# Kernel optimization log

Hardware: AMD Instinct MI355X
Metric: run time of the kernel (lower is better)

Reference implementation:

```python
import jax, jax.numpy as jnp
import numpy as np

N, Tq, Tk = 4096, 48, 48
E, H = 64, 4
HD = E // H
TN = 288            # time_num (5-min slots per day)
FE = 4              # forward_expansion
EPS = 1e-5


def _ln(x, g, b):
    mu = jnp.mean(x, axis=-1, keepdims=True)
    var = jnp.var(x, axis=-1, keepdims=True)
    return (x - mu) * jax.lax.rsqrt(var + EPS) * g + b


def setup_inputs() -> dict:
    rng = jax.random.key(0)
    ks = jax.random.split(rng, 12)
    s = 0.05
    return {
        "value": jax.random.normal(ks[0], (N, Tk, E), jnp.float32),
        "keys": jax.random.normal(ks[1], (N, Tk, E), jnp.float32),
        "query": jax.random.normal(ks[2], (N, Tq, E), jnp.float32),
        "Wv": jax.random.normal(ks[3], (HD, HD), jnp.float32) * s,
        "Wk": jax.random.normal(ks[4], (HD, HD), jnp.float32) * s,
        "Wq": jax.random.normal(ks[5], (HD, HD), jnp.float32) * s,
        "Wo": jax.random.normal(ks[6], (E, E), jnp.float32) * s,
        "bo": jnp.zeros((E,), jnp.float32),
        "temb": jax.random.normal(ks[7], (TN, E), jnp.float32) * s,
        "ln1_g": jnp.ones((E,), jnp.float32),
        "ln1_b": jnp.zeros((E,), jnp.float32),
        "ln2_g": jnp.ones((E,), jnp.float32),
        "ln2_b": jnp.zeros((E,), jnp.float32),
        "W1": jax.random.normal(ks[8], (FE * E, E), jnp.float32) * s,  # torch Linear(E, FE*E).weight
        "b1": jnp.zeros((FE * E,), jnp.float32),
        "W2": jax.random.normal(ks[9], (E, FE * E), jnp.float32) * s,
        "b2": jnp.zeros((E,), jnp.float32),
        "tq": 10,
    }


def reference(value, keys, query, Wv, Wk, Wq, Wo, bo, temb,
              ln1_g, ln1_b, ln2_g, ln2_b, W1, b1, W2, b2, tq):
    # temporal embedding add (tk = tq since tk=-1 default)
    tq_inds = (TN + tq + jnp.arange(Tq)) % TN
    tk_inds = (TN + tq + jnp.arange(Tk)) % TN
    q = query + temb[tq_inds][None, :, :]   # (N,Tq,E)
    k = keys + temb[tk_inds][None, :, :]    # (N,Tk,E)

    qh = q.reshape(N, Tq, H, HD)
    kh = k.reshape(N, Tk, H, HD)
    vh = value.reshape(N, Tk, H, HD)
    # per-head small linear projections (x @ W.T, no bias)
    qh = jnp.einsum('nthd,ed->nthe', qh, Wq)
    kh = jnp.einsum('nthd,ed->nthe', kh, Wk)
    vh = jnp.einsum('nthd,ed->nthe', vh, Wv)

    energy = jnp.einsum('nqhd,nkhd->nqkh', qh, kh)  # (N,Tq,Tk,H)
    # causal mask (mask=True path): masked entries set to -1e6 BEFORE scale+clamp
    tmask = jnp.tril(jnp.ones((Tq, Tk), jnp.float32))
    energy = jnp.where(tmask[None, :, :, None] == 0, jnp.float32(-1e6), energy)
    logits = jnp.clip(energy / jnp.float32(np.sqrt(E)), -5.0, 5.0)
    attention = jax.nn.softmax(logits, axis=2)       # softmax over k

    out = jnp.einsum('nqkh,nkhd->nqhd', attention, vh).reshape(N, Tq, E)
    out = out @ Wo.T + bo

    x = _ln(out + q, ln1_g, ln1_b)                   # dropout is identity (eval)
    ff = jax.nn.relu(x @ W1.T + b1) @ W2.T + b2
    return _ln(ff + x, ln2_g, ln2_b)
```

## Files before the change

kernel.cpp:

```cpp
#include <hip/hip_runtime.h>
#include <hip/hip_bf16.h>
#include <math.h>

#define NSEQ 4096
#define TN 288
#define EPSF 1e-5f

typedef short bf16x8 __attribute__((ext_vector_type(8)));
typedef float f32x4 __attribute__((ext_vector_type(4)));

#define WSV 0
#define WSK 256
#define WSQ 512
#define WSO 768
#define WS1 4864
#define WS2 21248

#define A_S   0
#define B_S   3456
#define C_S   6912
#define D_S   10496
#define CD_F  3456
#define H_S   6912

__device__ __forceinline__ unsigned short f2bf_u(float f) {
    __hip_bfloat16 h = __float2bfloat16(f);
    return *reinterpret_cast<const unsigned short*>(&h);
}
__device__ __forceinline__ unsigned int pk2(float a, float b) {
    return (unsigned int)f2bf_u(a) | ((unsigned int)f2bf_u(b) << 16);
}
__device__ __forceinline__ float bits2f(unsigned int u) { return __uint_as_float(u); }

__global__ void wconv_kernel(const float* __restrict__ Wv, const float* __restrict__ Wk,
                             const float* __restrict__ Wq, const float* __restrict__ Wo,
                             const float* __restrict__ W1, const float* __restrict__ W2,
                             short* __restrict__ ws) {
    int i = blockIdx.x * 256 + threadIdx.x;
    float v;
    if (i < 256)        v = Wv[i];
    else if (i < 512)   v = Wk[i - 256];
    else if (i < 768)   v = Wq[i - 512] * 0.125f;
    else if (i < 4864)  v = Wo[i - 768];
    else if (i < 21248) v = W1[i - 4864];
    else                v = W2[i - 21248];
    ws[i] = (short)f2bf_u(v);
}

__global__ __launch_bounds__(256, 5)
void ttrans_kernel(const float* __restrict__ value,
                   const float* __restrict__ keys,
                   const float* __restrict__ query,
                   const float* __restrict__ bo,
                   const float* __restrict__ temb,
                   const float* __restrict__ ln1g,
                   const float* __restrict__ ln1b,
                   const float* __restrict__ ln2g,
                   const float* __restrict__ ln2b,
                   const float* __restrict__ pb1,
                   const float* __restrict__ pb2,
                   const short* __restrict__ ws,
                   const int* __restrict__ tqp,
                   float* __restrict__ out)
{
    __shared__ __align__(16) unsigned char smem[27136];
    short* S16 = reinterpret_cast<short*>(smem);
    float* S32 = reinterpret_cast<float*>(smem);

    const int tid  = threadIdx.x;
    const int lane = tid & 63;
    const int w    = tid >> 6;
    const int l15  = lane & 15;
    const int lg   = lane >> 4;
    const int n    = blockIdx.x;
    const size_t gbase = (size_t)n * 3072;
    const int tqv  = *tqp;
    const int c4   = (lane & 15) * 4;
    const int rg   = lane >> 4;
    const int hh   = w;

    float4 qres4[3];
    {
        int t = w * 12 + rg;
        int ti = ((tqv % TN) + TN + t) % TN;
        #pragma unroll
        for (int it = 0; it < 3; ++it) {
            float4 tv = *reinterpret_cast<const float4*>(&temb[ti * 64 + c4]);
            float4 qv = *reinterpret_cast<const float4*>(&query[gbase + t * 64 + c4]);
            float4 kv = *reinterpret_cast<const float4*>(&keys [gbase + t * 64 + c4]);
            float4 vv = *reinterpret_cast<const float4*>(&value[gbase + t * 64 + c4]);
            float4 qq = make_float4(qv.x + tv.x, qv.y + tv.y, qv.z + tv.z, qv.w + tv.w);
            float4 kk = make_float4(kv.x + tv.x, kv.y + tv.y, kv.z + tv.z, kv.w + tv.w);
            qres4[it] = qq;
            *reinterpret_cast<uint2*>(&S16[A_S + t * 72 + c4]) =
                make_uint2(pk2(qq.x, qq.y), pk2(qq.z, qq.w));
            *reinterpret_cast<uint2*>(&S16[B_S + t * 72 + c4]) =
                make_uint2(pk2(kk.x, kk.y), pk2(kk.z, kk.w));
            *reinterpret_cast<uint2*>(&S16[C_S + t * 72 + c4]) =
                make_uint2(pk2(vv.x, vv.y), pk2(vv.z, vv.w));
            t += 4; ti += 4; if (ti >= TN) ti -= TN;
        }
    }
    __syncthreads();

    {
        bf16x8 bWv = {}, bWk = {}, bWq = {};
        if (lane < 32) {
            bWv = *reinterpret_cast<const bf16x8*>(&ws[WSV + l15 * 16 + lg * 8]);
            bWk = *reinterpret_cast<const bf16x8*>(&ws[WSK + l15 * 16 + lg * 8]);
            bWq = *reinterpret_cast<const bf16x8*>(&ws[WSQ + l15 * 16 + lg * 8]);
        }
        #pragma unroll
        for (int rt = 0; rt < 3; ++rt) {
            bf16x8 aQ = {}, aK = {}, aV = {};
            if (lane < 32) {
                int ro = (rt * 16 + l15) * 72 + hh * 16 + lg * 8;
                aQ = *reinterpret_cast<const bf16x8*>(&S16[A_S + ro]);
                aK = *reinterpret_cast<const bf16x8*>(&S16[B_S + ro]);
                aV = *reinterpret_cast<const bf16x8*>(&S16[C_S + ro]);
            }
            f32x4 z = {0.f,0.f,0.f,0.f};
            f32x4 cQ = __builtin_amdgcn_mfma_f32_16x16x32_bf16(aQ, bWq, z, 0, 0, 0);
            f32x4 cK = __builtin_amdgcn_mfma_f32_16x16x32_bf16(aK, bWk, z, 0, 0, 0);
            f32x4 cV = __builtin_amdgcn_mfma_f32_16x16x32_bf16(aV, bWv, z, 0, 0, 0);
            #pragma unroll
            for (int r = 0; r < 4; ++r) {
                int row = rt * 16 + lg * 4 + r;
                S16[A_S + row * 72 + hh * 16 + l15] = (short)f2bf_u(cQ[r]);
                S16[B_S + row * 72 + hh * 16 + l15] = (short)f2bf_u(cK[r]);
                S16[D_S + (hh * 16 + l15) * 48 + row] = (short)f2bf_u(cV[r]);
            }
        }
    }

    {
        const float PEXP = 0.006737946999085467f;
        const unsigned short PBF = f2bf_u(PEXP);
        bf16x8 bK0 = {}, bK1 = {}, bK2 = {};
        if (lane < 32) {
            bK0 = *reinterpret_cast<const bf16x8*>(&S16[B_S + ( 0 + l15) * 72 + hh * 16 + lg * 8]);
            bK1 = *reinterpret_cast<const bf16x8*>(&S16[B_S + (16 + l15) * 72 + hh * 16 + lg * 8]);
            bK2 = *reinterpret_cast<const bf16x8*>(&S16[B_S + (32 + l15) * 72 + hh * 16 + lg * 8]);
        }
        bf16x8 vA = *reinterpret_cast<const bf16x8*>(&S16[D_S + (hh * 16 + l15) * 48 + lg * 8]);
        bf16x8 vB = {};
        if (lane < 32)
            vB = *reinterpret_cast<const bf16x8*>(&S16[D_S + (hh * 16 + l15) * 48 + 32 + lg * 8]);
        asm volatile("" ::: "memory");

        const int abase = D_S + hh * 768;
        #pragma unroll
        for (int rt = 0; rt < 3; ++rt) {
            bf16x8 aQ = {};
            if (lane < 32)
                aQ = *reinterpret_cast<const bf16x8*>(&S16[A_S + (rt * 16 + l15) * 72 + hh * 16 + lg * 8]);
            f32x4 z = {0.f,0.f,0.f,0.f};
            f32x4 e0 = __builtin_amdgcn_mfma_f32_16x16x32_bf16(aQ, bK0, z, 0, 0, 0);
            f32x4 e1 = z, e2 = z;
            if (rt >= 1) e1 = __builtin_amdgcn_mfma_f32_16x16x32_bf16(aQ, bK1, z, 0, 0, 0);
            if (rt == 2) e2 = __builtin_amdgcn_mfma_f32_16x16x32_bf16(aQ, bK2, z, 0, 0, 0);
            float inv[4];
            #pragma unroll
            for (int r = 0; r < 4; ++r) {
                int tl = lg * 4 + r;
                int t = rt * 16 + tl;
                float p0, p1, p2;
                float v0 = fminf(5.f, fmaxf(-5.f, e0[r]));
                if (rt == 0) v0 = (l15 <= t) ? v0 : -5.f;
                p0 = __expf(v0);
                S16[abase + tl * 48 + l15] = (short)f2bf_u(p0);
                if (rt == 0) {
                    p1 = PEXP;
                    S16[abase + tl * 48 + 16 + l15] = (short)PBF;
                } else {
                    float v1 = fminf(5.f, fmaxf(-5.f, e1[r]));
                    if (rt == 1) v1 = (16 + l15 <= t) ? v1 : -5.f;
                    p1 = __expf(v1);
                    S16[abase + tl * 48 + 16 + l15] = (short)f2bf_u(p1);
                }
                if (rt < 2) {
                    p2 = PEXP;
                    S16[abase + tl * 48 + 32 + l15] = (short)PBF;
                } else {
                    float v2c = fminf(5.f, fmaxf(-5.f, e2[r]));
                    v2c = (32 + l15 <= t) ? v2c : -5.f;
                    p2 = __expf(v2c);
                    S16[abase + tl * 48 + 32 + l15] = (short)f2bf_u(p2);
                }
                float s = p0 + p1 + p2;
                s += __shfl_xor(s, 1);
                s += __shfl_xor(s, 2);
                s += __shfl_xor(s, 4);
                s += __shfl_xor(s, 8);
                inv[r] = __builtin_amdgcn_rcpf(s);
            }
            bf16x8 a0 = *reinterpret_cast<const bf16x8*>(&S16[abase + l15 * 48 + lg * 8]);
            bf16x8 a1 = {};
            if (lane < 32)
                a1 = *reinterpret_cast<const bf16x8*>(&S16[abase + l15 * 48 + 32 + lg * 8]);
            f32x4 zz = {0.f,0.f,0.f,0.f};
            f32x4 oc = __builtin_amdgcn_mfma_f32_16x16x32_bf16(a0, vA, zz, 0, 0, 0);
            oc = __builtin_amdgcn_mfma_f32_16x16x32_bf16(a1, vB, oc, 0, 0, 0);
            #pragma unroll
            for (int r = 0; r < 4; ++r)
                S16[B_S + (rt * 16 + lg * 4 + r) * 72 + hh * 16 + l15] =
                    (short)f2bf_u(oc[r] * inv[r]);
        }
    }
    __syncthreads();

    {
        bf16x8 bO0 = *reinterpret_cast<const bf16x8*>(&ws[WSO + (w * 16 + l15) * 64 + lg * 8]);
        bf16x8 bO1 = *reinterpret_cast<const bf16x8*>(&ws[WSO + (w * 16 + l15) * 64 + 32 + lg * 8]);
        const float bo_v = bo[w * 16 + l15];
        #pragma unroll
        for (int mt = 0; mt < 3; ++mt) {
            bf16x8 a0 = *reinterpret_cast<const bf16x8*>(&S16[B_S + (mt * 16 + l15) * 72 + lg * 8]);
            bf16x8 a1 = *reinterpret_cast<const bf16x8*>(&S16[B_S + (mt * 16 + l15) * 72 + 32 + lg * 8]);
            f32x4 c = {0.f,0.f,0.f,0.f};
            c = __builtin_amdgcn_mfma_f32_16x16x32_bf16(a0, bO0, c, 0, 0, 0);
            c = __builtin_amdgcn_mfma_f32_16x16x32_bf16(a1, bO1, c, 0, 0, 0);
            #pragma unroll
            for (int r = 0; r < 4; ++r)
                S32[CD_F + (mt * 16 + lg * 4 + r) * 68 + w * 16 + l15] = c[r] + bo_v;
        }
    }
    __syncthreads();

    {
        float4 g1 = *reinterpret_cast<const float4*>(&ln1g[c4]);
        float4 be1 = *reinterpret_cast<const float4*>(&ln1b[c4]);
        #pragma unroll
        for (int it = 0; it < 3; ++it) {
            int t = w * 12 + it * 4 + rg;
            float4 o = *reinterpret_cast<const float4*>(&S32[CD_F + t * 68 + c4]);
            float v0 = o.x + qres4[it].x, v1 = o.y + qres4[it].y;
            float v2 = o.z + qres4[it].z, v3 = o.w + qres4[it].w;
            float s1 = (v0 + v1) + (v2 + v3);
            float s2 = (v0 * v0 + v1 * v1) + (v2 * v2 + v3 * v3);
            s1 += __shfl_xor(s1, 1); s1 += __shfl_xor(s1, 2);
            s1 += __shfl_xor(s1, 4); s1 += __shfl_xor(s1, 8);
            s2 += __shfl_xor(s2, 1); s2 += __shfl_xor(s2, 2);
            s2 += __shfl_xor(s2, 4); s2 += __shfl_xor(s2, 8);
            float mu  = s1 * (1.f / 64.f);
            float var = s2 * (1.f / 64.f) - mu * mu;
            float rs = __builtin_amdgcn_rsqf(var + EPSF);
            float x0 = (v0 - mu) * rs * g1.x + be1.x;
            float x1 = (v1 - mu) * rs * g1.y + be1.y;
            float x2 = (v2 - mu) * rs * g1.z + be1.z;
            float x3 = (v3 - mu) * rs * g1.w + be1.w;
            *reinterpret_cast<uint2*>(&S16[A_S + t * 72 + c4]) =
                make_uint2(pk2(x0, x1), pk2(x2, x3));
        }
    }
    __syncthreads();

    f32x4 ffC[3];
    #pragma unroll
    for (int mt = 0; mt < 3; ++mt) ffC[mt] = (f32x4){0.f,0.f,0.f,0.f};

    #pragma unroll
    for (int hb = 0; hb < 2; ++hb) {
        #pragma unroll
        for (int jj = 0; jj < 2; ++jj) {
            int j16 = w * 2 + jj;
            int jrow = (hb * 8 + j16) * 16 + l15;
            bf16x8 b0 = *reinterpret_cast<const bf16x8*>(&ws[WS1 + jrow * 64 + lg * 8]);
            bf16x8 b1 = *reinterpret_cast<const bf16x8*>(&ws[WS1 + jrow * 64 + 32 + lg * 8]);
            float b1v = pb1[jrow];
            #pragma unroll
            for (int mt = 0; mt < 3; ++mt) {
                bf16x8 a0 = *reinterpret_cast<const bf16x8*>(&S16[A_S + (mt * 16 + l15) * 72 + lg * 8]);
                bf16x8 a1 = *reinterpret_cast<const bf16x8*>(&S16[A_S + (mt * 16 + l15) * 72 + 32 + lg * 8]);
                f32x4 c = {0.f,0.f,0.f,0.f};
                c = __builtin_amdgcn_mfma_f32_16x16x32_bf16(a0, b0, c, 0, 0, 0);
                c = __builtin_amdgcn_mfma_f32_16x16x32_bf16(a1, b1, c, 0, 0, 0);
                #pragma unroll
                for (int r = 0; r < 4; ++r)
                    S16[H_S + (mt * 16 + lg * 4 + r) * 136 + j16 * 16 + l15] =
                        (short)f2bf_u(fmaxf(c[r] + b1v, 0.f));
            }
        }
        __syncthreads();

        {
            const int wb = WS2 + (w * 16 + l15) * 256 + hb * 128;
            bf16x8 bw0 = *reinterpret_cast<const bf16x8*>(&ws[wb +  0 + lg * 8]);
            bf16x8 bw1 = *reinterpret_cast<const bf16x8*>(&ws[wb + 32 + lg * 8]);
            bf16x8 bw2 = *reinterpret_cast<const bf16x8*>(&ws[wb + 64 + lg * 8]);
            bf16x8 bw3 = *reinterpret_cast<const bf16x8*>(&ws[wb + 96 + lg * 8]);
            #pragma unroll
            for (int mt = 0; mt < 3; ++mt) {
                bf16x8 a0 = *reinterpret_cast<const bf16x8*>(&S16[H_S + (mt * 16 + l15) * 136 +  0 + lg * 8]);
                bf16x8 a1 = *reinterpret_cast<const bf16x8*>(&S16[H_S + (mt * 16 + l15) * 136 + 32 + lg * 8]);
                bf16x8 a2 = *reinterpret_cast<const bf16x8*>(&S16[H_S + (mt * 16 + l15) * 136 + 64 + lg * 8]);
                bf16x8 a3 = *reinterpret_cast<const bf16x8*>(&S16[H_S + (mt * 16 + l15) * 136 + 96 + lg * 8]);
                ffC[mt] = __builtin_amdgcn_mfma_f32_16x16x32_bf16(a0, bw0, ffC[mt], 0, 0, 0);
                ffC[mt] = __builtin_amdgcn_mfma_f32_16x16x32_bf16(a1, bw1, ffC[mt], 0, 0, 0);
                ffC[mt] = __builtin_amdgcn_mfma_f32_16x16x32_bf16(a2, bw2, ffC[mt], 0, 0, 0);
                ffC[mt] = __builtin_amdgcn_mfma_f32_16x16x32_bf16(a3, bw3, ffC[mt], 0, 0, 0);
            }
        }
        if (hb == 0) __syncthreads();
    }

    {
        float b2v = pb2[w * 16 + l15];
        #pragma unroll
        for (int mt = 0; mt < 3; ++mt)
            #pragma unroll
            for (int r = 0; r < 4; ++r)
                S16[B_S + (mt * 16 + lg * 4 + r) * 72 + w * 16 + l15] =
                    (short)f2bf_u(ffC[mt][r] + b2v);
    }
    __syncthreads();

    {
        float4 g2 = *reinterpret_cast<const float4*>(&ln2g[c4]);
        float4 be2 = *reinterpret_cast<const float4*>(&ln2b[c4]);
        #pragma unroll
        for (int it = 0; it < 3; ++it) {
            int t = w * 12 + it * 4 + rg;
            uint2 fp = *reinterpret_cast<const uint2*>(&S16[B_S + t * 72 + c4]);
            uint2 xp = *reinterpret_cast<const uint2*>(&S16[A_S + t * 72 + c4]);
            float v0 = bits2f(fp.x << 16) + bits2f(xp.x << 16);
            float v1 = bits2f(fp.x & 0xffff0000u) + bits2f(xp.x & 0xffff0000u);
            float v2 = bits2f(fp.y << 16) + bits2f(xp.y << 16);
            float v3 = bits2f(fp.y & 0xffff0000u) + bits2f(xp.y & 0xffff0000u);
            float s1 = (v0 + v1) + (v2 + v3);
            float s2 = (v0 * v0 + v1 * v1) + (v2 * v2 + v3 * v3);
            s1 += __shfl_xor(s1, 1); s1 += __shfl_xor(s1, 2);
            s1 += __shfl_xor(s1, 4); s1 += __shfl_xor(s1, 8);
            s2 += __shfl_xor(s2, 1); s2 += __shfl_xor(s2, 2);
            s2 += __shfl_xor(s2, 4); s2 += __shfl_xor(s2, 8);
            float mu  = s1 * (1.f / 64.f);
            float var = s2 * (1.f / 64.f) - mu * mu;
            float rs = __builtin_amdgcn_rsqf(var + EPSF);
            float y0 = (v0 - mu) * rs * g2.x + be2.x;
            float y1 = (v1 - mu) * rs * g2.y + be2.y;
            float y2 = (v2 - mu) * rs * g2.z + be2.z;
            float y3 = (v3 - mu) * rs * g2.w + be2.w;
            *reinterpret_cast<float4*>(&out[gbase + t * 64 + c4]) =
                make_float4(y0, y1, y2, y3);
        }
    }
}

extern "C" void kernel_launch(void* const* d_in, const int* in_sizes, int n_in,
                              void* d_out, int out_size, void* d_ws, size_t ws_size,
                              hipStream_t stream) {
    const float* value = (const float*)d_in[0];
    const float* keys  = (const float*)d_in[1];
    const float* query = (const float*)d_in[2];
    const float* Wv    = (const float*)d_in[3];
    const float* Wk    = (const float*)d_in[4];
    const float* Wq    = (const float*)d_in[5];
    const float* Wo    = (const float*)d_in[6];
    const float* bo    = (const float*)d_in[7];
    const float* temb  = (const float*)d_in[8];
    const float* ln1g  = (const float*)d_in[9];
    const float* ln1b  = (const float*)d_in[10];
    const float* ln2g  = (const float*)d_in[11];
    const float* ln2b  = (const float*)d_in[12];
    const float* W1    = (const float*)d_in[13];
    const float* b1    = (const float*)d_in[14];
    const float* W2    = (const float*)d_in[15];
    const float* b2    = (const float*)d_in[16];
    const int*   tq    = (const int*)d_in[17];
    float* outp = (float*)d_out;
    short* ws = (short*)d_ws;

    hipLaunchKernelGGL(wconv_kernel, dim3(147), dim3(256), 0, stream,
                       Wv, Wk, Wq, Wo, W1, W2, ws);
    hipLaunchKernelGGL(ttrans_kernel, dim3(NSEQ), dim3(256), 0, stream,
                       value, keys, query, bo, temb,
                       ln1g, ln1b, ln2g, ln2b, b1, b2, ws, tq, outp);
}
```

Baseline: 76.86 us.

## Shrink LDS footprint to raise occupancy by loading V directly into registers

Value rows are now loaded from global memory straight into registers in MFMA operand layout, which removes the C_S staging buffer. The output-projection result is stored as bf16 instead of fp32, and the LDS regions are re-aliased so shared memory drops from about 27KB to about 20KB. The launch bound is raised from 5 to 7 blocks per SIMD to exploit the smaller footprint. In exchange the bf16 rounding of the attention-projection output adds precision loss, an extra barrier is added, and the tighter register budget risks spills.

```diff
diff --git a/kernel.cpp b/kernel.cpp
--- a/kernel.cpp
+++ b/kernel.cpp
@@ -8,6 +8,7 @@
 
 typedef short bf16x8 __attribute__((ext_vector_type(8)));
 typedef float f32x4 __attribute__((ext_vector_type(4)));
+typedef unsigned int u32x4 __attribute__((ext_vector_type(4)));
 
 #define WSV 0
 #define WSK 256
@@ -18,10 +19,9 @@
 
 #define A_S   0
 #define B_S   3456
-#define C_S   6912
-#define D_S   10496
-#define CD_F  3456
-#define H_S   6912
+#define D_S   6912
+#define H_S   3456
+#define F_S   3456
 
 __device__ __forceinline__ unsigned short f2bf_u(float f) {
     __hip_bfloat16 h = __float2bfloat16(f);
@@ -31,6 +31,12 @@
     return (unsigned int)f2bf_u(a) | ((unsigned int)f2bf_u(b) << 16);
 }
 __device__ __forceinline__ float bits2f(unsigned int u) { return __uint_as_float(u); }
+__device__ __forceinline__ bf16x8 mk8(float4 a, float4 b) {
+    u32x4 u;
+    u.x = pk2(a.x, a.y); u.y = pk2(a.z, a.w);
+    u.z = pk2(b.x, b.y); u.w = pk2(b.z, b.w);
+    return __builtin_bit_cast(bf16x8, u);
+}
 
 __global__ void wconv_kernel(const float* __restrict__ Wv, const float* __restrict__ Wk,
                              const float* __restrict__ Wq, const float* __restrict__ Wo,
@@ -47,7 +53,7 @@
     ws[i] = (short)f2bf_u(v);
 }
 
-__global__ __launch_bounds__(256, 5)
+__global__ __launch_bounds__(256, 7)
 void ttrans_kernel(const float* __restrict__ value,
                    const float* __restrict__ keys,
                    const float* __restrict__ query,
@@ -63,9 +69,8 @@
                    const int* __restrict__ tqp,
                    float* __restrict__ out)
 {
-    __shared__ __align__(16) unsigned char smem[27136];
+    __shared__ __align__(16) unsigned char smem[19968];
     short* S16 = reinterpret_cast<short*>(smem);
-    float* S32 = reinterpret_cast<float*>(smem);
 
     const int tid  = threadIdx.x;
     const int lane = tid & 63;
@@ -79,6 +84,18 @@
     const int rg   = lane >> 4;
     const int hh   = w;
 
+    float4 vg0[3], vg1[3];
+    #pragma unroll
+    for (int rt = 0; rt < 3; ++rt) { vg0[rt] = make_float4(0,0,0,0); vg1[rt] = make_float4(0,0,0,0); }
+    if (lane < 32) {
+        #pragma unroll
+        for (int rt = 0; rt < 3; ++rt) {
+            const float* vp = &value[gbase + (rt * 16 + l15) * 64 + hh * 16 + lg * 8];
+            vg0[rt] = *reinterpret_cast<const float4*>(vp);
+            vg1[rt] = *reinterpret_cast<const float4*>(vp + 4);
+        }
+    }
+
     float4 qres4[3];
     {
         int t = w * 12 + rg;
@@ -88,7 +105,6 @@
             float4 tv = *reinterpret_cast<const float4*>(&temb[ti * 64 + c4]);
             float4 qv = *reinterpret_cast<const float4*>(&query[gbase + t * 64 + c4]);
             float4 kv = *reinterpret_cast<const float4*>(&keys [gbase + t * 64 + c4]);
-            float4 vv = *reinterpret_cast<const float4*>(&value[gbase + t * 64 + c4]);
             float4 qq = make_float4(qv.x + tv.x, qv.y + tv.y, qv.z + tv.z, qv.w + tv.w);
             float4 kk = make_float4(kv.x + tv.x, kv.y + tv.y, kv.z + tv.z, kv.w + tv.w);
             qres4[it] = qq;
@@ -96,8 +112,6 @@
                 make_uint2(pk2(qq.x, qq.y), pk2(qq.z, qq.w));
             *reinterpret_cast<uint2*>(&S16[B_S + t * 72 + c4]) =
                 make_uint2(pk2(kk.x, kk.y), pk2(kk.z, kk.w));
-            *reinterpret_cast<uint2*>(&S16[C_S + t * 72 + c4]) =
-                make_uint2(pk2(vv.x, vv.y), pk2(vv.z, vv.w));
             t += 4; ti += 4; if (ti >= TN) ti -= TN;
         }
     }
@@ -117,7 +131,7 @@
                 int ro = (rt * 16 + l15) * 72 + hh * 16 + lg * 8;
                 aQ = *reinterpret_cast<const bf16x8*>(&S16[A_S + ro]);
                 aK = *reinterpret_cast<const bf16x8*>(&S16[B_S + ro]);
-                aV = *reinterpret_cast<const bf16x8*>(&S16[C_S + ro]);
+                aV = mk8(vg0[rt], vg1[rt]);
             }
             f32x4 z = {0.f,0.f,0.f,0.f};
             f32x4 cQ = __builtin_amdgcn_mfma_f32_16x16x32_bf16(aQ, bWq, z, 0, 0, 0);
@@ -222,7 +236,8 @@
             c = __builtin_amdgcn_mfma_f32_16x16x32_bf16(a1, bO1, c, 0, 0, 0);
             #pragma unroll
             for (int r = 0; r < 4; ++r)
-                S32[CD_F + (mt * 16 + lg * 4 + r) * 68 + w * 16 + l15] = c[r] + bo_v;
+                S16[D_S + (mt * 16 + lg * 4 + r) * 64 + w * 16 + l15] =
+                    (short)f2bf_u(c[r] + bo_v);
         }
     }
     __syncthreads();
@@ -233,9 +248,11 @@
         #pragma unroll
         for (int it = 0; it < 3; ++it) {
             int t = w * 12 + it * 4 + rg;
-            float4 o = *reinterpret_cast<const float4*>(&S32[CD_F + t * 68 + c4]);
-            float v0 = o.x + qres4[it].x, v1 = o.y + qres4[it].y;
-            float v2 = o.z + qres4[it].z, v3 = o.w + qres4[it].w;
+            uint2 o2 = *reinterpret_cast<const uint2*>(&S16[D_S + t * 64 + c4]);
+            float v0 = bits2f(o2.x << 16) + qres4[it].x;
+            float v1 = bits2f(o2.x & 0xffff0000u) + qres4[it].y;
+            float v2 = bits2f(o2.y << 16) + qres4[it].z;
+            float v3 = bits2f(o2.y & 0xffff0000u) + qres4[it].w;
             float s1 = (v0 + v1) + (v2 + v3);
             float s2 = (v0 * v0 + v1 * v1) + (v2 * v2 + v3 * v3);
             s1 += __shfl_xor(s1, 1); s1 += __shfl_xor(s1, 2);
@@ -303,6 +320,7 @@
         }
         if (hb == 0) __syncthreads();
     }
+    __syncthreads();
 
     {
         float b2v = pb2[w * 16 + l15];
@@ -310,7 +328,7 @@
         for (int mt = 0; mt < 3; ++mt)
             #pragma unroll
             for (int r = 0; r < 4; ++r)
-                S16[B_S + (mt * 16 + lg * 4 + r) * 72 + w * 16 + l15] =
+                S16[F_S + (mt * 16 + lg * 4 + r) * 72 + w * 16 + l15] =
                     (short)f2bf_u(ffC[mt][r] + b2v);
     }
     __syncthreads();
@@ -321,7 +339,7 @@
         #pragma unroll
         for (int it = 0; it < 3; ++it) {
             int t = w * 12 + it * 4 + rg;
-            uint2 fp = *reinterpret_cast<const uint2*>(&S16[B_S + t * 72 + c4]);
+            uint2 fp = *reinterpret_cast<const uint2*>(&S16[F_S + t * 72 + c4]);
             uint2 xp = *reinterpret_cast<const uint2*>(&S16[A_S + t * 72 + c4]);
             float v0 = bits2f(fp.x << 16) + bits2f(xp.x << 16);
             float v1 = bits2f(fp.x & 0xffff0000u) + bits2f(xp.x & 0xffff0000u);
```

After: 96.48 us. +25.5%, slower.
